# Kernel optimization log

Measured on AMD Instinct MI355X. Metric: run time of the kernel, lower is better.

## Reference

```python
import jax, jax.numpy as jnp
import numpy as np

N = 3072      # num topics / nodes
D_IN = 64     # topic_dim
HID = 128     # hidden_dim
NH = 4        # n_heads
HD = HID // NH
L = 2         # n_gat_layers
B = 1024      # batch of topic_ids
ALPHA = 0.2   # leaky relu slope
TD = 0.1      # time decay
EPS = 1e-5    # layernorm eps


def setup_inputs() -> dict:
    key = jax.random.key(0)
    ks = jax.random.split(key, 16)
    rn = lambda k, s, sc=0.05: (jax.random.normal(k, s, jnp.float32) * sc)
    return {
        "topic_ids": jax.random.randint(ks[0], (B,), 0, N, dtype=jnp.int32),
        "adj_matrix": jax.random.randint(ks[1], (N, N), 0, 2).astype(jnp.float32),
        "time_matrix": jax.random.uniform(ks[2], (N, N), dtype=jnp.float32),
        "attractiveness": jax.random.normal(ks[3], (B,), jnp.float32),
        "topic_emb": rn(ks[4], (N, D_IN), 0.1),
        "Ws": rn(ks[5], (D_IN, HID)), "bs": jnp.zeros((HID,), jnp.float32),
        "Wa": rn(ks[6], (1, HID)), "ba": jnp.zeros((HID,), jnp.float32),
        "gat_W": rn(ks[7], (L, NH, HID, HD)),
        "gat_a": rn(ks[8], (L, NH, 2 * HD, 1)),
        "ln_g": jnp.ones((L, HID), jnp.float32),
        "ln_b": jnp.zeros((L, HID), jnp.float32),
        "W1": rn(ks[9], (HID, HID)), "b1": jnp.zeros((HID,), jnp.float32),
        "W2": rn(ks[10], (HID, 1)), "b2": jnp.zeros((1,), jnp.float32),
    }


def _gat_layer(x, adj, tmat, W, a, g, b):
    # x: [1, N, HID], adj/tmat: [N, N], W: [NH, HID, HD], a: [NH, 2*HD, 1]
    time_weights = jnp.exp(-TD * (tmat.max() - tmat))          # [N, N]
    h = jnp.einsum('bni,hio->bhno', x, W)                      # [1, NH, N, HD]
    a_src, a_dst = a[:, :HD, 0], a[:, HD:, 0]                  # [NH, HD]
    e_src = jnp.einsum('bhnd,hd->bhn', h, a_src)               # [1, NH, N]
    e_dst = jnp.einsum('bhnd,hd->bhn', h, a_dst)
    e = e_src[:, :, :, None] + e_dst[:, :, None, :]            # [1, NH, N, N]
    e = jax.nn.leaky_relu(e, ALPHA) * time_weights[None, None]
    mask = adj[None, None]                                     # [1, 1, N, N]
    e = jnp.where(mask == 0, -jnp.inf, e)
    has_nb = mask.sum(axis=-1) > 0                             # [1, 1, N]
    e = jnp.where(has_nb[..., None], e, 0.0)                   # isolated rows -> zeros -> uniform softmax (matches torch)
    att = jax.nn.softmax(e, axis=-1)
    att = jnp.where(jnp.isnan(att), 0.0, att)
    out = jnp.einsum('bhij,bhjo->bhio', att, h)                # [1, NH, N, HD]
    out = out.transpose(0, 2, 1, 3).reshape(1, N, NH * HD)
    out = jax.nn.elu(out)
    mu = out.mean(axis=-1, keepdims=True)
    var = out.var(axis=-1, keepdims=True)
    return (out - mu) / jnp.sqrt(var + EPS) * g + b


def reference(topic_ids, adj_matrix, time_matrix, attractiveness, topic_emb,
              Ws, bs, Wa, ba, gat_W, gat_a, ln_g, ln_b, W1, b1, W2, b2):
    struct = topic_emb @ Ws + bs                               # [N, HID]
    attract = attractiveness[:, None] @ Wa + ba                # [B, HID]
    x = struct[None]                                           # [1, N, HID]
    for l in range(L):
        x = _gat_layer(x, adj_matrix, time_matrix, gat_W[l], gat_a[l], ln_g[l], ln_b[l])
    topic_feats = x[0][topic_ids]                              # [B, HID]
    hidden = jax.nn.relu((topic_feats + attract) @ W1 + b1)
    return hidden @ W2 + b2                                    # [B, 1]
```

## Files before the change

kernel.cpp:

```cpp
#include <hip/hip_runtime.h>

#define N 3072
#define D_IN 64
#define HID 128
#define NH 4
#define HD 32
#define NB 1024
#define ALPHA 0.2f
#define TD 0.1f
#define EPS 1e-5f
#define LOG2E 1.4426950408889634f
#define TSPLIT 16
#define JSPAN (N / TSPLIT)
#define NCH (JSPAN / 64)
#define PSTR 72

typedef unsigned int uint;
typedef unsigned short ushort;
typedef __attribute__((ext_vector_type(8))) __bf16 bf16x8;
typedef __attribute__((ext_vector_type(4))) float f32x4;

__device__ __forceinline__ ushort f2bf(float f) {
  union { float f; uint u; } c; c.f = f;
  uint u = c.u;
  return (ushort)((u + 0x7FFFu + ((u >> 16) & 1u)) >> 16);
}
__device__ __forceinline__ float bf2f(ushort u) {
  union { uint u; float f; } c; c.u = ((uint)u) << 16;
  return c.f;
}

__global__ __launch_bounds__(256) void k_prep(const float* __restrict__ tmat,
                                              const float* __restrict__ adj,
                                              const float* __restrict__ gW,
                                              uint* __restrict__ tmax_u,
                                              uint* __restrict__ deg0,
                                              ushort* __restrict__ wt) {
  int t = threadIdx.x;
  if (blockIdx.x >= N / 4) {
    int l = blockIdx.x - N / 4;
    const float* gWl = gW + (size_t)l * NH * HID * HD;
    ushort* wtl = wt + (size_t)l * HID * HID;
    int n = t >> 1, k0 = (t & 1) * 64;
    int h = n >> 5, o = n & 31;
    const float* src = gWl + (size_t)h * (HID * HD) + o;
    ushort* dst = wtl + (size_t)n * HID + k0;
#pragma unroll
    for (int kk = 0; kk < 64; kk += 8) {
      ushort v[8];
#pragma unroll
      for (int j = 0; j < 8; j++) v[j] = f2bf(src[(size_t)(k0 + kk + j) * HD]);
      uint4 pk;
      pk.x = (uint)v[0] | ((uint)v[1] << 16);
      pk.y = (uint)v[2] | ((uint)v[3] << 16);
      pk.z = (uint)v[4] | ((uint)v[5] << 16);
      pk.w = (uint)v[6] | ((uint)v[7] << 16);
      *(uint4*)&dst[kk] = pk;
    }
    return;
  }
  int row = blockIdx.x * 4 + (t >> 6);
  int lane = t & 63;
  const float4* tr = (const float4*)(tmat + (size_t)row * N);
  const float4* ar = (const float4*)(adj + (size_t)row * N);
  float mx = 0.f, s = 0.f;
#pragma unroll
  for (int it = 0; it < 12; it++) {
    float4 t4 = tr[lane + it * 64];
    float4 a4 = ar[lane + it * 64];
    mx = fmaxf(mx, fmaxf(fmaxf(t4.x, t4.y), fmaxf(t4.z, t4.w)));
    s += a4.x + a4.y + a4.z + a4.w;
  }
  for (int o = 32; o > 0; o >>= 1) { mx = fmaxf(mx, __shfl_xor(mx, o)); s += __shfl_xor(s, o); }
  __shared__ float smx[4];
  int w = t >> 6;
  if (lane == 0) { deg0[row] = (s == 0.f) ? 1u : 0u; smx[w] = mx; }
  __syncthreads();
  if (t == 0) {
    float m = fmaxf(fmaxf(smx[0], smx[1]), fmaxf(smx[2], smx[3]));
    atomicMax(tmax_u, __float_as_uint(m));
  }
}

__global__ __launch_bounds__(256) void k_hx(int layer,
                                            const float* __restrict__ emb,
                                            const float* __restrict__ Ws,
                                            const float* __restrict__ bs,
                                            const float* __restrict__ o_part,
                                            const float* __restrict__ s_part,
                                            const float* __restrict__ lg,
                                            const float* __restrict__ lb,
                                            const ushort* __restrict__ wt,
                                            const float* __restrict__ gA,
                                            ushort* __restrict__ hT,
                                            float* __restrict__ es,
                                            float* __restrict__ ed) {
  __shared__ __align__(16) ushort wlds[HID][136];
  __shared__ __align__(16) ushort xs2[16][17][8];
  __shared__ __align__(16) float embs[16][D_IN];
  int t = threadIdx.x;
  int n0 = blockIdx.x * 16;
  int r = t >> 4, q = t & 15, c0 = q * 8;

  if (layer == 0) {
    float* wsf = (float*)&wlds[0][0];
    const float4* Ws4 = (const float4*)Ws;
    float4* wsf4 = (float4*)wsf;
#pragma unroll
    for (int j = 0; j < 8; j++) wsf4[t + j * 256] = Ws4[t + j * 256];
    ((float4*)&embs[0][0])[t] = ((const float4*)(emb + (size_t)n0 * D_IN))[t];
    __syncthreads();
    float acc[8];
    float4 b0 = *(const float4*)&bs[c0];
    float4 b1 = *(const float4*)&bs[c0 + 4];
    acc[0] = b0.x; acc[1] = b0.y; acc[2] = b0.z; acc[3] = b0.w;
    acc[4] = b1.x; acc[5] = b1.y; acc[6] = b1.z; acc[7] = b1.w;
    for (int i = 0; i < D_IN; i++) {
      float ev = embs[r][i];
      float4 w0 = *(const float4*)&wsf[i * HID + c0];
      float4 w1 = *(const float4*)&wsf[i * HID + c0 + 4];
      acc[0] += ev * w0.x; acc[1] += ev * w0.y; acc[2] += ev * w0.z; acc[3] += ev * w0.w;
      acc[4] += ev * w1.x; acc[5] += ev * w1.y; acc[6] += ev * w1.z; acc[7] += ev * w1.w;
    }
    uint4 pk;
    pk.x = (uint)f2bf(acc[0]) | ((uint)f2bf(acc[1]) << 16);
    pk.y = (uint)f2bf(acc[2]) | ((uint)f2bf(acc[3]) << 16);
    pk.z = (uint)f2bf(acc[4]) | ((uint)f2bf(acc[5]) << 16);
    pk.w = (uint)f2bf(acc[6]) | ((uint)f2bf(acc[7]) << 16);
    __syncthreads();
    *(uint4*)&xs2[q][r][0] = pk;
    const uint4* wt4 = (const uint4*)wt;
#pragma unroll
    for (int j = 0; j < 8; j++) {
      int ci = t + j * 256;
      *(uint4*)&wlds[ci >> 4][(ci & 15) * 8] = wt4[ci];
    }
    __syncthreads();
  } else {
    const uint4* wt4 = (const uint4*)wt;
#pragma unroll
    for (int j = 0; j < 8; j++) {
      int ci = t + j * 256;
      *(uint4*)&wlds[ci >> 4][(ci & 15) * 8] = wt4[ci];
    }
    int i = n0 + r;
    float ox[8] = {0.f, 0.f, 0.f, 0.f, 0.f, 0.f, 0.f, 0.f};
    float sden = 0.f;
#pragma unroll
    for (int sp = 0; sp < TSPLIT; sp++) {
      const float* op = o_part + ((size_t)sp * N + i) * HID + c0;
      float4 a = *(const float4*)op;
      float4 b = *(const float4*)(op + 4);
      ox[0] += a.x; ox[1] += a.y; ox[2] += a.z; ox[3] += a.w;
      ox[4] += b.x; ox[5] += b.y; ox[6] += b.z; ox[7] += b.w;
      sden += s_part[((size_t)sp * N + i) * NH + (c0 >> 5)];
    }
    float v[8], sm = 0.f, sq = 0.f;
#pragma unroll
    for (int j = 0; j < 8; j++) {
      float x = ox[j] / sden;
      x = x > 0.f ? x : expm1f(x);
      v[j] = x; sm += x; sq += x * x;
    }
    sm += __shfl_xor(sm, 1); sq += __shfl_xor(sq, 1);
    sm += __shfl_xor(sm, 2); sq += __shfl_xor(sq, 2);
    sm += __shfl_xor(sm, 4); sq += __shfl_xor(sq, 4);
    sm += __shfl_xor(sm, 8); sq += __shfl_xor(sq, 8);
    float mu = sm / (float)HID;
    float var = sq / (float)HID - mu * mu;
    float rs = rsqrtf(var + EPS);
    float4 g0 = *(const float4*)&lg[c0], g1 = *(const float4*)&lg[c0 + 4];
    float4 bb0 = *(const float4*)&lb[c0], bb1 = *(const float4*)&lb[c0 + 4];
    float xo[8];
    xo[0] = (v[0] - mu) * rs * g0.x + bb0.x; xo[1] = (v[1] - mu) * rs * g0.y + bb0.y;
    xo[2] = (v[2] - mu) * rs * g0.z + bb0.z; xo[3] = (v[3] - mu) * rs * g0.w + bb0.w;
    xo[4] = (v[4] - mu) * rs * g1.x + bb1.x; xo[5] = (v[5] - mu) * rs * g1.y + bb1.y;
    xo[6] = (v[6] - mu) * rs * g1.z + bb1.z; xo[7] = (v[7] - mu) * rs * g1.w + bb1.w;
    uint4 pk;
    pk.x = (uint)f2bf(xo[0]) | ((uint)f2bf(xo[1]) << 16);
    pk.y = (uint)f2bf(xo[2]) | ((uint)f2bf(xo[3]) << 16);
    pk.z = (uint)f2bf(xo[4]) | ((uint)f2bf(xo[5]) << 16);
    pk.w = (uint)f2bf(xo[6]) | ((uint)f2bf(xo[7]) << 16);
    *(uint4*)&xs2[q][r][0] = pk;
    __syncthreads();
  }

  int w = t >> 6, l = t & 63;
  int m = l & 15, g = l >> 4;
  f32x4 ac0 = {0.f, 0.f, 0.f, 0.f}, ac1 = {0.f, 0.f, 0.f, 0.f};
#pragma unroll
  for (int k0 = 0; k0 < 4; k0++) {
    bf16x8 afr = *(const bf16x8*)&xs2[k0 * 4 + g][m][0];
    bf16x8 bf0 = *(const bf16x8*)&wlds[w * 32 + m][k0 * 32 + g * 8];
    bf16x8 bf1 = *(const bf16x8*)&wlds[w * 32 + 16 + m][k0 * 32 + g * 8];
    ac0 = __builtin_amdgcn_mfma_f32_16x16x32_bf16(afr, bf0, ac0, 0, 0, 0);
    ac1 = __builtin_amdgcn_mfma_f32_16x16x32_bf16(afr, bf1, ac1, 0, 0, 0);
  }
  const float* aB = gA + w * 2 * HD;
  float as0 = aB[m], as1 = aB[16 + m];
  float ad0 = aB[HD + m], ad1 = aB[HD + 16 + m];
  float esv[4], edv[4];
#pragma unroll
  for (int qq = 0; qq < 4; qq++) {
    float h0 = ac0[qq], h1 = ac1[qq];
    float e_s = h0 * as0 + h1 * as1;
    float e_d = h0 * ad0 + h1 * ad1;
    e_s += __shfl_xor(e_s, 1); e_d += __shfl_xor(e_d, 1);
    e_s += __shfl_xor(e_s, 2); e_d += __shfl_xor(e_d, 2);
    e_s += __shfl_xor(e_s, 4); e_d += __shfl_xor(e_d, 4);
    e_s += __shfl_xor(e_s, 8); e_d += __shfl_xor(e_d, 8);
    esv[qq] = e_s; edv[qq] = e_d;
  }
  if (m == 0) {
    *(float4*)&es[(size_t)w * N + n0 + g * 4] = make_float4(esv[0], esv[1], esv[2], esv[3]);
    *(float4*)&ed[(size_t)w * N + n0 + g * 4] = make_float4(edv[0], edv[1], edv[2], edv[3]);
  }
  {
    uint2 p0, p1;
    p0.x = (uint)f2bf(ac0[0]) | ((uint)f2bf(ac0[1]) << 16);
    p0.y = (uint)f2bf(ac0[2]) | ((uint)f2bf(ac0[3]) << 16);
    p1.x = (uint)f2bf(ac1[0]) | ((uint)f2bf(ac1[1]) << 16);
    p1.y = (uint)f2bf(ac1[2]) | ((uint)f2bf(ac1[3]) << 16);
    *(uint2*)&hT[(size_t)(w * 32 + m) * N + n0 + g * 4] = p0;
    *(uint2*)&hT[(size_t)(w * 32 + 16 + m) * N + n0 + g * 4] = p1;
  }
}

__global__ __launch_bounds__(256) void k_att(const float* __restrict__ tmat,
                                             const float* __restrict__ adj,
                                             const uint* __restrict__ tmax_u,
                                             const ushort* __restrict__ hT,
                                             const float* __restrict__ es,
                                             const float* __restrict__ ed,
                                             const uint* __restrict__ deg0,
                                             float* __restrict__ o_part,
                                             float* __restrict__ s_part) {
  __shared__ __align__(16) ushort ps[2][NH][32][PSTR];
  int tid = threadIdx.x;
  int ib = blockIdx.x * 32;
  int sp = blockIdx.y;
  int jb0 = sp * JSPAN;
  float tmax = __uint_as_float(*tmax_u);
  const float c1 = TD * LOG2E;

  int jl = tid & 31;
  int ig = tid >> 5;
  float esr[4][NH];
  uint dg[4];
#pragma unroll
  for (int p = 0; p < 4; p++) {
    int i = ib + ig + 8 * p;
    dg[p] = deg0[i];
#pragma unroll
    for (int h_ = 0; h_ < NH; h_++) esr[p][h_] = es[h_ * N + i];
  }

  int wv = tid >> 6;
  int ln = tid & 63;
  f32x4 acc00 = {0.f, 0.f, 0.f, 0.f}, acc01 = {0.f, 0.f, 0.f, 0.f};
  f32x4 acc10 = {0.f, 0.f, 0.f, 0.f}, acc11 = {0.f, 0.f, 0.f, 0.f};
  float sacc[4][NH];
#pragma unroll
  for (int p = 0; p < 4; p++)
#pragma unroll
    for (int h_ = 0; h_ < NH; h_++) sacc[p][h_] = 0.f;

  float2 t2v[4], a2v[4], edv[NH];

  auto LOADS = [&](int ch) {
    int j0 = jb0 + ch * 64 + 2 * jl;
#pragma unroll
    for (int p = 0; p < 4; p++) {
      t2v[p] = *(const float2*)&tmat[(size_t)(ib + ig + 8 * p) * N + j0];
      a2v[p] = *(const float2*)&adj[(size_t)(ib + ig + 8 * p) * N + j0];
    }
#pragma unroll
    for (int h_ = 0; h_ < NH; h_++) edv[h_] = *(const float2*)&ed[h_ * N + j0];
  };
  auto COMPUTE = [&](int buf) {
#pragma unroll
    for (int p = 0; p < 4; p++) {
      float m0 = __builtin_amdgcn_exp2f(c1 * (t2v[p].x - tmax)) * LOG2E;
      float m1 = __builtin_amdgcn_exp2f(c1 * (t2v[p].y - tmax)) * LOG2E;
      bool z0 = (a2v[p].x != 0.f), z1 = (a2v[p].y != 0.f);
#pragma unroll
      for (int h_ = 0; h_ < NH; h_++) {
        float e0 = esr[p][h_] + edv[h_].x;
        float e1 = esr[p][h_] + edv[h_].y;
        float l0 = fmaxf(e0, 0.f) + ALPHA * fminf(e0, 0.f);
        float l1 = fmaxf(e1, 0.f) + ALPHA * fminf(e1, 0.f);
        float p0 = __builtin_amdgcn_exp2f(l0 * m0);
        float p1 = __builtin_amdgcn_exp2f(l1 * m1);
        p0 = z0 ? p0 : 0.f;
        p1 = z1 ? p1 : 0.f;
        if (dg[p]) { p0 = 1.f; p1 = 1.f; }
        sacc[p][h_] += p0 + p1;
        uint pk = (__float_as_uint(p0) >> 16) | (__float_as_uint(p1) & 0xFFFF0000u);
        *(uint*)&ps[buf][h_][ig + 8 * p][2 * jl] = pk;
      }
    }
  };

  LOADS(0);
  COMPUTE(0);

  int r = ln & 15, g = ln >> 4;
  for (int ch = 0; ch < NCH; ch++) {
    __syncthreads();
    if (ch + 1 < NCH) LOADS(ch + 1);
    {
      int jb = jb0 + ch * 64;
      const ushort* hTb = hT + (size_t)(wv * HD) * N + jb;
      int buf = ch & 1;
#pragma unroll
      for (int ks = 0; ks < 2; ks++) {
        bf16x8 a0f = *(const bf16x8*)&ps[buf][wv][r][ks * 32 + g * 8];
        bf16x8 a1f = *(const bf16x8*)&ps[buf][wv][16 + r][ks * 32 + g * 8];
        bf16x8 b0 = *(const bf16x8*)(hTb + (size_t)r * N + ks * 32 + g * 8);
        bf16x8 b1 = *(const bf16x8*)(hTb + (size_t)(16 + r) * N + ks * 32 + g * 8);
        acc00 = __builtin_amdgcn_mfma_f32_16x16x32_bf16(a0f, b0, acc00, 0, 0, 0);
        acc01 = __builtin_amdgcn_mfma_f32_16x16x32_bf16(a0f, b1, acc01, 0, 0, 0);
        acc10 = __builtin_amdgcn_mfma_f32_16x16x32_bf16(a1f, b0, acc10, 0, 0, 0);
        acc11 = __builtin_amdgcn_mfma_f32_16x16x32_bf16(a1f, b1, acc11, 0, 0, 0);
      }
    }
    if (ch + 1 < NCH) COMPUTE((ch + 1) & 1);
  }

#pragma unroll
  for (int p = 0; p < 4; p++)
#pragma unroll
    for (int h_ = 0; h_ < NH; h_++) {
      float v = sacc[p][h_];
      v += __shfl_xor(v, 16); v += __shfl_xor(v, 8);
      v += __shfl_xor(v, 4);  v += __shfl_xor(v, 2); v += __shfl_xor(v, 1);
      if (jl == 0) {
        int i = ib + ig + 8 * p;
        s_part[((size_t)sp * N + i) * NH + h_] = v;
      }
    }
  {
#pragma unroll
    for (int qq = 0; qq < 4; qq++) {
      int i0 = ib + g * 4 + qq;
      int i1 = ib + 16 + g * 4 + qq;
      float* op0 = o_part + ((size_t)sp * N + i0) * HID + wv * HD;
      float* op1 = o_part + ((size_t)sp * N + i1) * HID + wv * HD;
      op0[r] = acc00[qq];
      op0[16 + r] = acc01[qq];
      op1[r] = acc10[qq];
      op1[16 + r] = acc11[qq];
    }
  }
}

__global__ __launch_bounds__(256) void k_final(const float* __restrict__ o_part,
                                               const float* __restrict__ s_part,
                                               const float* __restrict__ lg,
                                               const float* __restrict__ lb,
                                               const int* __restrict__ tid,
                                               const float* __restrict__ attr,
                                               const float* __restrict__ Wa,
                                               const float* __restrict__ ba,
                                               const float* __restrict__ W1,
                                               const float* __restrict__ b1,
                                               const float* __restrict__ W2,
                                               const float* __restrict__ b2,
                                               float* __restrict__ out) {
  __shared__ __align__(16) float tf[16][HID];
  __shared__ __align__(16) ushort w1lds[HID * HID];
  int t = threadIdx.x;
  int r = t >> 4, q = t & 15, c0 = q * 8;
  int bI0 = blockIdx.x * 16;
  int id = tid[bI0 + r];
  float av = attr[bI0 + r];
  const float4* W14 = (const float4*)W1;
#pragma unroll
  for (int j = 0; j < 8; j++) {
    int ci = t + j * 256;
    float4 a = W14[ci * 2], b = W14[ci * 2 + 1];
    uint4 pk;
    pk.x = (uint)f2bf(a.x) | ((uint)f2bf(a.y) << 16);
    pk.y = (uint)f2bf(a.z) | ((uint)f2bf(a.w) << 16);
    pk.z = (uint)f2bf(b.x) | ((uint)f2bf(b.y) << 16);
    pk.w = (uint)f2bf(b.z) | ((uint)f2bf(b.w) << 16);
    *(uint4*)&w1lds[ci * 8] = pk;
  }
  float ox[8] = {0.f, 0.f, 0.f, 0.f, 0.f, 0.f, 0.f, 0.f};
  float sden = 0.f;
#pragma unroll
  for (int sp = 0; sp < TSPLIT; sp++) {
    const float* op = o_part + ((size_t)sp * N + id) * HID + c0;
    float4 a = *(const float4*)op;
    float4 b = *(const float4*)(op + 4);
    ox[0] += a.x; ox[1] += a.y; ox[2] += a.z; ox[3] += a.w;
    ox[4] += b.x; ox[5] += b.y; ox[6] += b.z; ox[7] += b.w;
    sden += s_part[((size_t)sp * N + id) * NH + (c0 >> 5)];
  }
  float v[8], sm = 0.f, sq = 0.f;
#pragma unroll
  for (int j = 0; j < 8; j++) {
    float x = ox[j] / sden;
    x = x > 0.f ? x : expm1f(x);
    v[j] = x; sm += x; sq += x * x;
  }
  sm += __shfl_xor(sm, 1); sq += __shfl_xor(sq, 1);
  sm += __shfl_xor(sm, 2); sq += __shfl_xor(sq, 2);
  sm += __shfl_xor(sm, 4); sq += __shfl_xor(sq, 4);
  sm += __shfl_xor(sm, 8); sq += __shfl_xor(sq, 8);
  float mu = sm / (float)HID;
  float var = sq / (float)HID - mu * mu;
  float rs = rsqrtf(var + EPS);
#pragma unroll
  for (int j = 0; j < 8; j++) {
    int c = c0 + j;
    tf[r][c] = (v[j] - mu) * rs * lg[c] + lb[c] + av * Wa[c] + ba[c];
  }
  __syncthreads();
  float hid[8];
  float4 bb0 = *(const float4*)&b1[c0], bb1 = *(const float4*)&b1[c0 + 4];
  hid[0] = bb0.x; hid[1] = bb0.y; hid[2] = bb0.z; hid[3] = bb0.w;
  hid[4] = bb1.x; hid[5] = bb1.y; hid[6] = bb1.z; hid[7] = bb1.w;
  for (int i = 0; i < HID; i++) {
    float tv = tf[r][i];
    uint4 wv = *(const uint4*)&w1lds[i * HID + c0];
    hid[0] += tv * bf2f((ushort)(wv.x & 0xFFFFu));
    hid[1] += tv * bf2f((ushort)(wv.x >> 16));
    hid[2] += tv * bf2f((ushort)(wv.y & 0xFFFFu));
    hid[3] += tv * bf2f((ushort)(wv.y >> 16));
    hid[4] += tv * bf2f((ushort)(wv.z & 0xFFFFu));
    hid[5] += tv * bf2f((ushort)(wv.z >> 16));
    hid[6] += tv * bf2f((ushort)(wv.w & 0xFFFFu));
    hid[7] += tv * bf2f((ushort)(wv.w >> 16));
  }
  float pr = 0.f;
#pragma unroll
  for (int j = 0; j < 8; j++) pr += fmaxf(hid[j], 0.f) * W2[c0 + j];
  pr += __shfl_xor(pr, 1);
  pr += __shfl_xor(pr, 2);
  pr += __shfl_xor(pr, 4);
  pr += __shfl_xor(pr, 8);
  if (q == 0) out[bI0 + r] = pr + b2[0];
}

extern "C" void kernel_launch(void* const* d_in, const int* in_sizes, int n_in,
                              void* d_out, int out_size, void* d_ws, size_t ws_size,
                              hipStream_t stream) {
  (void)in_sizes; (void)n_in; (void)out_size; (void)ws_size;
  const int*   topic_ids = (const int*)d_in[0];
  const float* adj  = (const float*)d_in[1];
  const float* tmat = (const float*)d_in[2];
  const float* attr = (const float*)d_in[3];
  const float* emb  = (const float*)d_in[4];
  const float* Ws   = (const float*)d_in[5];
  const float* bs   = (const float*)d_in[6];
  const float* Wa   = (const float*)d_in[7];
  const float* ba   = (const float*)d_in[8];
  const float* gW   = (const float*)d_in[9];
  const float* gA   = (const float*)d_in[10];
  const float* lng  = (const float*)d_in[11];
  const float* lnb  = (const float*)d_in[12];
  const float* W1   = (const float*)d_in[13];
  const float* b1   = (const float*)d_in[14];
  const float* W2   = (const float*)d_in[15];
  const float* b2   = (const float*)d_in[16];

  char* ws = (char*)d_ws;
  size_t o = 0;
  auto alloc = [&](size_t bytes) { void* p = ws + o; o += (bytes + 255) & ~255ull; return p; };
  uint*   tmax_u = (uint*)alloc(4);
  uint*   deg0   = (uint*)alloc((size_t)N * 4);
  ushort* hT     = (ushort*)alloc((size_t)HID * N * 2);
  float*  es     = (float*)alloc((size_t)NH * N * 4);
  float*  ed     = (float*)alloc((size_t)NH * N * 4);
  float*  o_part = (float*)alloc((size_t)TSPLIT * N * HID * 4);
  float*  s_part = (float*)alloc((size_t)TSPLIT * N * NH * 4);
  ushort* wt     = (ushort*)alloc((size_t)2 * HID * HID * 2);

  hipMemsetAsync(tmax_u, 0, 4, stream);
  k_prep<<<N / 4 + 2, 256, 0, stream>>>(tmat, adj, gW, tmax_u, deg0, wt);

  dim3 gr(N / 32, TSPLIT);
  k_hx<<<N / 16, 256, 0, stream>>>(0, emb, Ws, bs, nullptr, nullptr, nullptr, nullptr,
                                   wt, gA, hT, es, ed);
  k_att<<<gr, 256, 0, stream>>>(tmat, adj, tmax_u, hT, es, ed, deg0, o_part, s_part);
  k_hx<<<N / 16, 256, 0, stream>>>(1, nullptr, nullptr, nullptr, o_part, s_part, lng, lnb,
                                   wt + (size_t)HID * HID, gA + (size_t)NH * 2 * HD,
                                   hT, es, ed);
  k_att<<<gr, 256, 0, stream>>>(tmat, adj, tmax_u, hT, es, ed, deg0, o_part, s_part);
  k_final<<<NB / 16, 256, 0, stream>>>(o_part, s_part, lng + HID, lnb + HID,
                                       topic_ids, attr, Wa, ba, W1, b1, W2, b2, (float*)d_out);
}
```

Measured before the change: 220.4 us.

## Fuse prep into layer-0 projection kernel and halve attention column splits

Removes the separate prep kernel and memset. The row-max/degree scan and the bf16 weight transpose now run in the same launch as the layer-0 projection (extra blocks, with weights converted in-kernel). Each attention block reduces the per-row maxima itself instead of using a global atomicMax. TSPLIT drops from 16 to 8, which halves the partial-sum traffic and reduction work but gives the attention kernel half as many blocks. Every hx block now repeats the weight conversion, and the in-block loop also uses strided LDS stores.

```diff
diff --git a/kernel.cpp b/kernel.cpp
--- a/kernel.cpp
+++ b/kernel.cpp
@@ -10,7 +10,7 @@
 #define TD 0.1f
 #define EPS 1e-5f
 #define LOG2E 1.4426950408889634f
-#define TSPLIT 16
+#define TSPLIT 8
 #define JSPAN (N / TSPLIT)
 #define NCH (JSPAN / 64)
 #define PSTR 72
@@ -30,161 +30,29 @@
   return c.f;
 }
 
-__global__ __launch_bounds__(256) void k_prep(const float* __restrict__ tmat,
-                                              const float* __restrict__ adj,
-                                              const float* __restrict__ gW,
-                                              uint* __restrict__ tmax_u,
-                                              uint* __restrict__ deg0,
-                                              ushort* __restrict__ wt) {
-  int t = threadIdx.x;
-  if (blockIdx.x >= N / 4) {
-    int l = blockIdx.x - N / 4;
-    const float* gWl = gW + (size_t)l * NH * HID * HD;
-    ushort* wtl = wt + (size_t)l * HID * HID;
-    int n = t >> 1, k0 = (t & 1) * 64;
-    int h = n >> 5, o = n & 31;
-    const float* src = gWl + (size_t)h * (HID * HD) + o;
-    ushort* dst = wtl + (size_t)n * HID + k0;
-#pragma unroll
-    for (int kk = 0; kk < 64; kk += 8) {
-      ushort v[8];
-#pragma unroll
-      for (int j = 0; j < 8; j++) v[j] = f2bf(src[(size_t)(k0 + kk + j) * HD]);
-      uint4 pk;
-      pk.x = (uint)v[0] | ((uint)v[1] << 16);
-      pk.y = (uint)v[2] | ((uint)v[3] << 16);
-      pk.z = (uint)v[4] | ((uint)v[5] << 16);
-      pk.w = (uint)v[6] | ((uint)v[7] << 16);
-      *(uint4*)&dst[kk] = pk;
-    }
-    return;
-  }
-  int row = blockIdx.x * 4 + (t >> 6);
-  int lane = t & 63;
-  const float4* tr = (const float4*)(tmat + (size_t)row * N);
-  const float4* ar = (const float4*)(adj + (size_t)row * N);
-  float mx = 0.f, s = 0.f;
-#pragma unroll
-  for (int it = 0; it < 12; it++) {
-    float4 t4 = tr[lane + it * 64];
-    float4 a4 = ar[lane + it * 64];
-    mx = fmaxf(mx, fmaxf(fmaxf(t4.x, t4.y), fmaxf(t4.z, t4.w)));
-    s += a4.x + a4.y + a4.z + a4.w;
-  }
-  for (int o = 32; o > 0; o >>= 1) { mx = fmaxf(mx, __shfl_xor(mx, o)); s += __shfl_xor(s, o); }
-  __shared__ float smx[4];
-  int w = t >> 6;
-  if (lane == 0) { deg0[row] = (s == 0.f) ? 1u : 0u; smx[w] = mx; }
-  __syncthreads();
-  if (t == 0) {
-    float m = fmaxf(fmaxf(smx[0], smx[1]), fmaxf(smx[2], smx[3]));
-    atomicMax(tmax_u, __float_as_uint(m));
-  }
-}
-
-__global__ __launch_bounds__(256) void k_hx(int layer,
-                                            const float* __restrict__ emb,
-                                            const float* __restrict__ Ws,
-                                            const float* __restrict__ bs,
-                                            const float* __restrict__ o_part,
-                                            const float* __restrict__ s_part,
-                                            const float* __restrict__ lg,
-                                            const float* __restrict__ lb,
-                                            const ushort* __restrict__ wt,
-                                            const float* __restrict__ gA,
-                                            ushort* __restrict__ hT,
-                                            float* __restrict__ es,
-                                            float* __restrict__ ed) {
-  __shared__ __align__(16) ushort wlds[HID][136];
-  __shared__ __align__(16) ushort xs2[16][17][8];
-  __shared__ __align__(16) float embs[16][D_IN];
-  int t = threadIdx.x;
-  int n0 = blockIdx.x * 16;
-  int r = t >> 4, q = t & 15, c0 = q * 8;
-
-  if (layer == 0) {
-    float* wsf = (float*)&wlds[0][0];
-    const float4* Ws4 = (const float4*)Ws;
-    float4* wsf4 = (float4*)wsf;
-#pragma unroll
-    for (int j = 0; j < 8; j++) wsf4[t + j * 256] = Ws4[t + j * 256];
-    ((float4*)&embs[0][0])[t] = ((const float4*)(emb + (size_t)n0 * D_IN))[t];
-    __syncthreads();
-    float acc[8];
-    float4 b0 = *(const float4*)&bs[c0];
-    float4 b1 = *(const float4*)&bs[c0 + 4];
-    acc[0] = b0.x; acc[1] = b0.y; acc[2] = b0.z; acc[3] = b0.w;
-    acc[4] = b1.x; acc[5] = b1.y; acc[6] = b1.z; acc[7] = b1.w;
-    for (int i = 0; i < D_IN; i++) {
-      float ev = embs[r][i];
-      float4 w0 = *(const float4*)&wsf[i * HID + c0];
-      float4 w1 = *(const float4*)&wsf[i * HID + c0 + 4];
-      acc[0] += ev * w0.x; acc[1] += ev * w0.y; acc[2] += ev * w0.z; acc[3] += ev * w0.w;
-      acc[4] += ev * w1.x; acc[5] += ev * w1.y; acc[6] += ev * w1.z; acc[7] += ev * w1.w;
-    }
-    uint4 pk;
-    pk.x = (uint)f2bf(acc[0]) | ((uint)f2bf(acc[1]) << 16);
-    pk.y = (uint)f2bf(acc[2]) | ((uint)f2bf(acc[3]) << 16);
-    pk.z = (uint)f2bf(acc[4]) | ((uint)f2bf(acc[5]) << 16);
-    pk.w = (uint)f2bf(acc[6]) | ((uint)f2bf(acc[7]) << 16);
-    __syncthreads();
-    *(uint4*)&xs2[q][r][0] = pk;
-    const uint4* wt4 = (const uint4*)wt;
-#pragma unroll
-    for (int j = 0; j < 8; j++) {
-      int ci = t + j * 256;
-      *(uint4*)&wlds[ci >> 4][(ci & 15) * 8] = wt4[ci];
-    }
-    __syncthreads();
-  } else {
-    const uint4* wt4 = (const uint4*)wt;
-#pragma unroll
-    for (int j = 0; j < 8; j++) {
-      int ci = t + j * 256;
-      *(uint4*)&wlds[ci >> 4][(ci & 15) * 8] = wt4[ci];
-    }
-    int i = n0 + r;
-    float ox[8] = {0.f, 0.f, 0.f, 0.f, 0.f, 0.f, 0.f, 0.f};
-    float sden = 0.f;
-#pragma unroll
-    for (int sp = 0; sp < TSPLIT; sp++) {
-      const float* op = o_part + ((size_t)sp * N + i) * HID + c0;
-      float4 a = *(const float4*)op;
-      float4 b = *(const float4*)(op + 4);
-      ox[0] += a.x; ox[1] += a.y; ox[2] += a.z; ox[3] += a.w;
-      ox[4] += b.x; ox[5] += b.y; ox[6] += b.z; ox[7] += b.w;
-      sden += s_part[((size_t)sp * N + i) * NH + (c0 >> 5)];
-    }
-    float v[8], sm = 0.f, sq = 0.f;
-#pragma unroll
-    for (int j = 0; j < 8; j++) {
-      float x = ox[j] / sden;
-      x = x > 0.f ? x : expm1f(x);
-      v[j] = x; sm += x; sq += x * x;
-    }
-    sm += __shfl_xor(sm, 1); sq += __shfl_xor(sq, 1);
-    sm += __shfl_xor(sm, 2); sq += __shfl_xor(sq, 2);
-    sm += __shfl_xor(sm, 4); sq += __shfl_xor(sq, 4);
-    sm += __shfl_xor(sm, 8); sq += __shfl_xor(sq, 8);
-    float mu = sm / (float)HID;
-    float var = sq / (float)HID - mu * mu;
-    float rs = rsqrtf(var + EPS);
-    float4 g0 = *(const float4*)&lg[c0], g1 = *(const float4*)&lg[c0 + 4];
-    float4 bb0 = *(const float4*)&lb[c0], bb1 = *(const float4*)&lb[c0 + 4];
-    float xo[8];
-    xo[0] = (v[0] - mu) * rs * g0.x + bb0.x; xo[1] = (v[1] - mu) * rs * g0.y + bb0.y;
-    xo[2] = (v[2] - mu) * rs * g0.z + bb0.z; xo[3] = (v[3] - mu) * rs * g0.w + bb0.w;
-    xo[4] = (v[4] - mu) * rs * g1.x + bb1.x; xo[5] = (v[5] - mu) * rs * g1.y + bb1.y;
-    xo[6] = (v[6] - mu) * rs * g1.z + bb1.z; xo[7] = (v[7] - mu) * rs * g1.w + bb1.w;
-    uint4 pk;
-    pk.x = (uint)f2bf(xo[0]) | ((uint)f2bf(xo[1]) << 16);
-    pk.y = (uint)f2bf(xo[2]) | ((uint)f2bf(xo[3]) << 16);
-    pk.z = (uint)f2bf(xo[4]) | ((uint)f2bf(xo[5]) << 16);
-    pk.w = (uint)f2bf(xo[6]) | ((uint)f2bf(xo[7]) << 16);
-    *(uint4*)&xs2[q][r][0] = pk;
-    __syncthreads();
-  }
-
+__device__ __forceinline__ void stage_wt(const float* __restrict__ gWl,
+                                         ushort (*wlds)[136], int t) {
+  const float4* g4 = (const float4*)gWl;
+#pragma unroll
+  for (int j = 0; j < 16; j++) {
+    int f = t + j * 256;
+    float4 v = g4[f];
+    int h = f >> 10, kk = (f >> 3) & 127, o4 = (f & 7) * 4;
+    ushort* base = &wlds[(h << 5) + o4][kk];
+    base[0] = f2bf(v.x);
+    base[136] = f2bf(v.y);
+    base[272] = f2bf(v.z);
+    base[408] = f2bf(v.w);
+  }
+}
+
+__device__ __forceinline__ void hx_tail(const ushort (*wlds)[136],
+                                        const ushort (*xs2)[17][8],
+                                        const float* __restrict__ gA,
+                                        ushort* __restrict__ hT,
+                                        float* __restrict__ es,
+                                        float* __restrict__ ed,
+                                        int n0, int t) {
   int w = t >> 6, l = t & 63;
   int m = l & 15, g = l >> 4;
   f32x4 ac0 = {0.f, 0.f, 0.f, 0.f}, ac1 = {0.f, 0.f, 0.f, 0.f};
@@ -215,20 +83,144 @@
     *(float4*)&es[(size_t)w * N + n0 + g * 4] = make_float4(esv[0], esv[1], esv[2], esv[3]);
     *(float4*)&ed[(size_t)w * N + n0 + g * 4] = make_float4(edv[0], edv[1], edv[2], edv[3]);
   }
-  {
-    uint2 p0, p1;
-    p0.x = (uint)f2bf(ac0[0]) | ((uint)f2bf(ac0[1]) << 16);
-    p0.y = (uint)f2bf(ac0[2]) | ((uint)f2bf(ac0[3]) << 16);
-    p1.x = (uint)f2bf(ac1[0]) | ((uint)f2bf(ac1[1]) << 16);
-    p1.y = (uint)f2bf(ac1[2]) | ((uint)f2bf(ac1[3]) << 16);
-    *(uint2*)&hT[(size_t)(w * 32 + m) * N + n0 + g * 4] = p0;
-    *(uint2*)&hT[(size_t)(w * 32 + 16 + m) * N + n0 + g * 4] = p1;
-  }
+  uint2 p0, p1;
+  p0.x = (uint)f2bf(ac0[0]) | ((uint)f2bf(ac0[1]) << 16);
+  p0.y = (uint)f2bf(ac0[2]) | ((uint)f2bf(ac0[3]) << 16);
+  p1.x = (uint)f2bf(ac1[0]) | ((uint)f2bf(ac1[1]) << 16);
+  p1.y = (uint)f2bf(ac1[2]) | ((uint)f2bf(ac1[3]) << 16);
+  *(uint2*)&hT[(size_t)(w * 32 + m) * N + n0 + g * 4] = p0;
+  *(uint2*)&hT[(size_t)(w * 32 + 16 + m) * N + n0 + g * 4] = p1;
+}
+
+__global__ __launch_bounds__(256) void k_hx0p(const float* __restrict__ tmat,
+                                              const float* __restrict__ adj,
+                                              const float* __restrict__ emb,
+                                              const float* __restrict__ Ws,
+                                              const float* __restrict__ bs,
+                                              const float* __restrict__ gW,
+                                              const float* __restrict__ gA,
+                                              ushort* __restrict__ hT,
+                                              float* __restrict__ es,
+                                              float* __restrict__ ed,
+                                              float* __restrict__ rowmax,
+                                              uint* __restrict__ deg0) {
+  int t = threadIdx.x;
+  if (blockIdx.x >= N / 16) {
+    int row = (blockIdx.x - N / 16) * 4 + (t >> 6);
+    int lane = t & 63;
+    const float4* tr = (const float4*)(tmat + (size_t)row * N);
+    const float4* ar = (const float4*)(adj + (size_t)row * N);
+    float mx = 0.f, s = 0.f;
+#pragma unroll
+    for (int it = 0; it < 12; it++) {
+      float4 t4 = tr[lane + it * 64];
+      float4 a4 = ar[lane + it * 64];
+      mx = fmaxf(mx, fmaxf(fmaxf(t4.x, t4.y), fmaxf(t4.z, t4.w)));
+      s += a4.x + a4.y + a4.z + a4.w;
+    }
+    for (int o = 32; o > 0; o >>= 1) { mx = fmaxf(mx, __shfl_xor(mx, o)); s += __shfl_xor(s, o); }
+    if (lane == 0) { rowmax[row] = mx; deg0[row] = (s == 0.f) ? 1u : 0u; }
+    return;
+  }
+  __shared__ __align__(16) ushort wlds[HID][136];
+  __shared__ __align__(16) ushort xs2[16][17][8];
+  __shared__ __align__(16) float embs[16][D_IN];
+  int n0 = blockIdx.x * 16;
+  int r = t >> 4, q = t & 15, c0 = q * 8;
+
+  float* wsf = (float*)&wlds[0][0];
+  const float4* Ws4 = (const float4*)Ws;
+  float4* wsf4 = (float4*)wsf;
+#pragma unroll
+  for (int j = 0; j < 8; j++) wsf4[t + j * 256] = Ws4[t + j * 256];
+  ((float4*)&embs[0][0])[t] = ((const float4*)(emb + (size_t)n0 * D_IN))[t];
+  __syncthreads();
+  float acc[8];
+  float4 b0 = *(const float4*)&bs[c0];
+  float4 b1 = *(const float4*)&bs[c0 + 4];
+  acc[0] = b0.x; acc[1] = b0.y; acc[2] = b0.z; acc[3] = b0.w;
+  acc[4] = b1.x; acc[5] = b1.y; acc[6] = b1.z; acc[7] = b1.w;
+  for (int i = 0; i < D_IN; i++) {
+    float ev = embs[r][i];
+    float4 w0 = *(const float4*)&wsf[i * HID + c0];
+    float4 w1 = *(const float4*)&wsf[i * HID + c0 + 4];
+    acc[0] += ev * w0.x; acc[1] += ev * w0.y; acc[2] += ev * w0.z; acc[3] += ev * w0.w;
+    acc[4] += ev * w1.x; acc[5] += ev * w1.y; acc[6] += ev * w1.z; acc[7] += ev * w1.w;
+  }
+  uint4 pk;
+  pk.x = (uint)f2bf(acc[0]) | ((uint)f2bf(acc[1]) << 16);
+  pk.y = (uint)f2bf(acc[2]) | ((uint)f2bf(acc[3]) << 16);
+  pk.z = (uint)f2bf(acc[4]) | ((uint)f2bf(acc[5]) << 16);
+  pk.w = (uint)f2bf(acc[6]) | ((uint)f2bf(acc[7]) << 16);
+  __syncthreads();
+  *(uint4*)&xs2[q][r][0] = pk;
+  stage_wt(gW, wlds, t);
+  __syncthreads();
+  hx_tail(wlds, xs2, gA, hT, es, ed, n0, t);
+}
+
+__global__ __launch_bounds__(256) void k_hx1(const float* __restrict__ o_part,
+                                             const float* __restrict__ s_part,
+                                             const float* __restrict__ lg,
+                                             const float* __restrict__ lb,
+                                             const float* __restrict__ gW1,
+                                             const float* __restrict__ gA,
+                                             ushort* __restrict__ hT,
+                                             float* __restrict__ es,
+                                             float* __restrict__ ed) {
+  __shared__ __align__(16) ushort wlds[HID][136];
+  __shared__ __align__(16) ushort xs2[16][17][8];
+  int t = threadIdx.x;
+  int n0 = blockIdx.x * 16;
+  int r = t >> 4, q = t & 15, c0 = q * 8;
+
+  stage_wt(gW1, wlds, t);
+  int i = n0 + r;
+  float ox[8] = {0.f, 0.f, 0.f, 0.f, 0.f, 0.f, 0.f, 0.f};
+  float sden = 0.f;
+#pragma unroll
+  for (int sp = 0; sp < TSPLIT; sp++) {
+    const float* op = o_part + ((size_t)sp * N + i) * HID + c0;
+    float4 a = *(const float4*)op;
+    float4 b = *(const float4*)(op + 4);
+    ox[0] += a.x; ox[1] += a.y; ox[2] += a.z; ox[3] += a.w;
+    ox[4] += b.x; ox[5] += b.y; ox[6] += b.z; ox[7] += b.w;
+    sden += s_part[((size_t)sp * N + i) * NH + (c0 >> 5)];
+  }
+  float v[8], sm = 0.f, sq = 0.f;
+#pragma unroll
+  for (int j = 0; j < 8; j++) {
+    float x = ox[j] / sden;
+    x = x > 0.f ? x : expm1f(x);
+    v[j] = x; sm += x; sq += x * x;
+  }
+  sm += __shfl_xor(sm, 1); sq += __shfl_xor(sq, 1);
+  sm += __shfl_xor(sm, 2); sq += __shfl_xor(sq, 2);
+  sm += __shfl_xor(sm, 4); sq += __shfl_xor(sq, 4);
+  sm += __shfl_xor(sm, 8); sq += __shfl_xor(sq, 8);
+  float mu = sm / (float)HID;
+  float var = sq / (float)HID - mu * mu;
+  float rs = rsqrtf(var + EPS);
+  float4 g0 = *(const float4*)&lg[c0], g1 = *(const float4*)&lg[c0 + 4];
+  float4 bb0 = *(const float4*)&lb[c0], bb1 = *(const float4*)&lb[c0 + 4];
+  float xo[8];
+  xo[0] = (v[0] - mu) * rs * g0.x + bb0.x; xo[1] = (v[1] - mu) * rs * g0.y + bb0.y;
+  xo[2] = (v[2] - mu) * rs * g0.z + bb0.z; xo[3] = (v[3] - mu) * rs * g0.w + bb0.w;
+  xo[4] = (v[4] - mu) * rs * g1.x + bb1.x; xo[5] = (v[5] - mu) * rs * g1.y + bb1.y;
+  xo[6] = (v[6] - mu) * rs * g1.z + bb1.z; xo[7] = (v[7] - mu) * rs * g1.w + bb1.w;
+  uint4 pk;
+  pk.x = (uint)f2bf(xo[0]) | ((uint)f2bf(xo[1]) << 16);
+  pk.y = (uint)f2bf(xo[2]) | ((uint)f2bf(xo[3]) << 16);
+  pk.z = (uint)f2bf(xo[4]) | ((uint)f2bf(xo[5]) << 16);
+  pk.w = (uint)f2bf(xo[6]) | ((uint)f2bf(xo[7]) << 16);
+  *(uint4*)&xs2[q][r][0] = pk;
+  __syncthreads();
+  hx_tail(wlds, xs2, gA, hT, es, ed, n0, t);
 }
 
 __global__ __launch_bounds__(256) void k_att(const float* __restrict__ tmat,
                                              const float* __restrict__ adj,
-                                             const uint* __restrict__ tmax_u,
+                                             const float* __restrict__ rowmax,
                                              const ushort* __restrict__ hT,
                                              const float* __restrict__ es,
                                              const float* __restrict__ ed,
@@ -236,12 +228,22 @@
                                              float* __restrict__ o_part,
                                              float* __restrict__ s_part) {
   __shared__ __align__(16) ushort ps[2][NH][32][PSTR];
+  __shared__ float redl[4];
   int tid = threadIdx.x;
   int ib = blockIdx.x * 32;
   int sp = blockIdx.y;
   int jb0 = sp * JSPAN;
-  float tmax = __uint_as_float(*tmax_u);
   const float c1 = TD * LOG2E;
+
+  {
+    float m = 0.f;
+#pragma unroll
+    for (int j = 0; j < 12; j++) m = fmaxf(m, rowmax[tid + j * 256]);
+    for (int o = 32; o > 0; o >>= 1) m = fmaxf(m, __shfl_xor(m, o));
+    if ((tid & 63) == 0) redl[tid >> 6] = m;
+  }
+  __syncthreads();
+  float tmax = fmaxf(fmaxf(redl[0], redl[1]), fmaxf(redl[2], redl[3]));
 
   int jl = tid & 31;
   int ig = tid >> 5;
@@ -468,26 +470,22 @@
   char* ws = (char*)d_ws;
   size_t o = 0;
   auto alloc = [&](size_t bytes) { void* p = ws + o; o += (bytes + 255) & ~255ull; return p; };
-  uint*   tmax_u = (uint*)alloc(4);
+  float*  rowmax = (float*)alloc((size_t)N * 4);
   uint*   deg0   = (uint*)alloc((size_t)N * 4);
   ushort* hT     = (ushort*)alloc((size_t)HID * N * 2);
   float*  es     = (float*)alloc((size_t)NH * N * 4);
   float*  ed     = (float*)alloc((size_t)NH * N * 4);
   float*  o_part = (float*)alloc((size_t)TSPLIT * N * HID * 4);
   float*  s_part = (float*)alloc((size_t)TSPLIT * N * NH * 4);
-  ushort* wt     = (ushort*)alloc((size_t)2 * HID * HID * 2);
-
-  hipMemsetAsync(tmax_u, 0, 4, stream);
-  k_prep<<<N / 4 + 2, 256, 0, stream>>>(tmat, adj, gW, tmax_u, deg0, wt);
 
   dim3 gr(N / 32, TSPLIT);
-  k_hx<<<N / 16, 256, 0, stream>>>(0, emb, Ws, bs, nullptr, nullptr, nullptr, nullptr,
-                                   wt, gA, hT, es, ed);
-  k_att<<<gr, 256, 0, stream>>>(tmat, adj, tmax_u, hT, es, ed, deg0, o_part, s_part);
-  k_hx<<<N / 16, 256, 0, stream>>>(1, nullptr, nullptr, nullptr, o_part, s_part, lng, lnb,
-                                   wt + (size_t)HID * HID, gA + (size_t)NH * 2 * HD,
-                                   hT, es, ed);
-  k_att<<<gr, 256, 0, stream>>>(tmat, adj, tmax_u, hT, es, ed, deg0, o_part, s_part);
+  k_hx0p<<<N / 16 + N / 4, 256, 0, stream>>>(tmat, adj, emb, Ws, bs, gW, gA,
+                                             hT, es, ed, rowmax, deg0);
+  k_att<<<gr, 256, 0, stream>>>(tmat, adj, rowmax, hT, es, ed, deg0, o_part, s_part);
+  k_hx1<<<N / 16, 256, 0, stream>>>(o_part, s_part, lng, lnb,
+                                    gW + (size_t)NH * HID * HD, gA + (size_t)NH * 2 * HD,
+                                    hT, es, ed);
+  k_att<<<gr, 256, 0, stream>>>(tmat, adj, rowmax, hT, es, ed, deg0, o_part, s_part);
   k_final<<<NB / 16, 256, 0, stream>>>(o_part, s_part, lng + HID, lnb + HID,
                                        topic_ids, attr, Wa, ba, W1, b1, W2, b2, (float*)d_out);
 }
```

Result: faster. 200.5 us (-9.0%).
